# Performance work log

Measured on AMD Instinct MI355X. Metric: run time of the kernel, lower is better.

Reference implementation:

```python
import jax, jax.numpy as jnp
import numpy as np

B, S, H = 8, 1024, 1024
NH, HD = 16, 64
LN_EPS = 1e-12


def setup_inputs() -> dict:
    key = jax.random.key(0)
    ks = jax.random.split(key, 8)
    sd = 0.02
    return {
        "hidden_states": jax.random.normal(ks[0], (B, S, H), jnp.float32),
        "attention_mask": jnp.zeros((B, 1, 1, S), jnp.float32),
        "Wq": jax.random.normal(ks[1], (H, H), jnp.float32) * sd,
        "bq": jnp.zeros((H,), jnp.float32),
        "Wk": jax.random.normal(ks[2], (H, H), jnp.float32) * sd,
        "bk": jnp.zeros((H,), jnp.float32),
        "Wv": jax.random.normal(ks[3], (H, H), jnp.float32) * sd,
        "bv": jnp.zeros((H,), jnp.float32),
        "Wo": jax.random.normal(ks[4], (H, H), jnp.float32) * sd,
        "bo": jnp.zeros((H,), jnp.float32),
        "ln_gamma": jnp.ones((H,), jnp.float32),
        "ln_beta": jnp.zeros((H,), jnp.float32),
    }


def _heads(x):
    # [B,S,H] -> [B,NH,S,HD]
    return x.reshape(B, S, NH, HD).transpose(0, 2, 1, 3)


def reference(hidden_states, attention_mask, Wq, bq, Wk, bk, Wv, bv, Wo, bo, ln_gamma, ln_beta):
    # QKV projections (torch Linear: x @ W.T + b)
    q = _heads(hidden_states @ Wq.T + bq)
    k = _heads(hidden_states @ Wk.T + bk)
    v = _heads(hidden_states @ Wv.T + bv)
    # scaled dot-product attention with additive mask
    scores = jnp.einsum("bhqd,bhkd->bhqk", q, k) / np.sqrt(HD).astype(np.float32)
    scores = scores + attention_mask  # broadcast [B,1,1,S]
    probs = jax.nn.softmax(scores, axis=-1)
    ctx = jnp.einsum("bhqk,bhkd->bhqd", probs, v)
    ctx = ctx.transpose(0, 2, 1, 3).reshape(B, S, H)
    # output projection + residual + LayerNorm
    out = ctx @ Wo.T + bo
    x = out + hidden_states
    mu = jnp.mean(x, axis=-1, keepdims=True)
    var = jnp.var(x, axis=-1, keepdims=True)
    return (x - mu) * jax.lax.rsqrt(var + LN_EPS) * ln_gamma + ln_beta
```

## Files before the change

### kernel.cpp

```cpp
#include <hip/hip_runtime.h>
#include <stdint.h>

typedef __attribute__((ext_vector_type(8))) __bf16 bf16x8;
typedef __attribute__((ext_vector_type(8))) unsigned short ushortx8;
typedef __attribute__((ext_vector_type(4))) unsigned short ushortx4;
typedef __attribute__((ext_vector_type(4))) short short4v;
typedef __attribute__((ext_vector_type(4))) float floatx4;

#define LOG2E 1.4426950408889634f
#define QSCALE 0.18033688011112043f

#define ASYNC16(g, l) __builtin_amdgcn_global_load_lds( \
    (__attribute__((address_space(1))) void*)(g),       \
    (__attribute__((address_space(3))) void*)(l), 16, 0, 0)

__device__ __forceinline__ unsigned short f2bf(float f) {
    unsigned int u = __float_as_uint(f);
    u += 0x7fffu + ((u >> 16) & 1u);
    return (unsigned short)(u >> 16);
}
__device__ __forceinline__ float bf2f(unsigned short u) {
    return __uint_as_float((unsigned)u << 16);
}

__device__ __forceinline__ floatx4 mfma32(bf16x8 a, bf16x8 b, floatx4 c) {
    return __builtin_amdgcn_mfma_f32_16x16x32_bf16(a, b, c, 0, 0, 0);
}
__device__ __forceinline__ floatx4 mfma16(short4v a, short4v b, floatx4 c) {
    return __builtin_amdgcn_mfma_f32_16x16x16bf16_1k(a, b, c, 0, 0, 0);
}

__global__ __launch_bounds__(256) void cvt_all(
    const float* __restrict__ hidden,
    const float* __restrict__ Wq, const float* __restrict__ Wk,
    const float* __restrict__ Wv, const float* __restrict__ Wo,
    unsigned short* __restrict__ hid_bf,
    unsigned short* __restrict__ oqkv, unsigned short* __restrict__ oo)
{
    const float* src;
    unsigned short* dst;
    int i;
    if (blockIdx.x < 4096) {
        src = hidden; dst = hid_bf;
        i = blockIdx.x * 256 + threadIdx.x;
    } else {
        int blk = (blockIdx.x - 4096) >> 9;
        src = (blk == 0) ? Wq : (blk == 1) ? Wk : (blk == 2) ? Wv : Wo;
        dst = (blk == 3) ? oo : oqkv + (size_t)blk * 1048576;
        i = ((blockIdx.x - 4096) & 511) * 256 + threadIdx.x;
    }
    const float4* p = (const float4*)src + (size_t)i * 2;
    float4 a = p[0], b = p[1];
    ushortx8 o;
    o[0] = f2bf(a.x); o[1] = f2bf(a.y); o[2] = f2bf(a.z); o[3] = f2bf(a.w);
    o[4] = f2bf(b.x); o[5] = f2bf(b.y); o[6] = f2bf(b.z); o[7] = f2bf(b.w);
    *((ushortx8*)dst + i) = o;
}

template<bool SWAP>
__device__ __forceinline__ void kloop_dbuf(
    const unsigned short* __restrict__ Ag,
    const unsigned short* __restrict__ Wg,
    unsigned short As[2][8192], unsigned short Bs[2][8192],
    int wm, int wn, int l16, int quad, int t,
    floatx4 acc[4][4])
{
    const int t8 = t * 8;
#define SAx(bf_, i_, kt_) ASYNC16(Ag + (size_t)(i_) * 32 * 1024 + (kt_) * 64, &As[bf_][(i_) * 2048 + t8])
#define SBx(bf_, i_, kt_) ASYNC16(Wg + (size_t)(i_) * 32 * 1024 + (kt_) * 64, &Bs[bf_][(i_) * 2048 + t8])
#pragma unroll
    for (int i = 0; i < 4; i++) { SAx(0, i, 0); SBx(0, i, 0); }
    __syncthreads();

#pragma unroll 1
    for (int kt = 0; kt < 16; ++kt) {
        const int cur = kt & 1, nb = cur ^ 1;
        if (kt < 15) {
#pragma unroll
            for (int i = 0; i < 4; i++) { SAx(nb, i, kt + 1); SBx(nb, i, kt + 1); }
        }
#pragma unroll
        for (int s = 0; s < 2; s++) {
            int pb = ((s * 4 + quad) ^ (l16 & 7)) * 8;
            bf16x8 af[4], bfr[4];
#pragma unroll
            for (int mt = 0; mt < 4; mt++)
                af[mt] = *(const bf16x8*)(&As[cur][(wm + mt * 16 + l16) * 64 + pb]);
#pragma unroll
            for (int nt = 0; nt < 4; nt++)
                bfr[nt] = *(const bf16x8*)(&Bs[cur][(wn + nt * 16 + l16) * 64 + pb]);
            if (SWAP) {
#pragma unroll
                for (int ft = 0; ft < 4; ft++)
#pragma unroll
                    for (int st = 0; st < 4; st++)
                        acc[ft][st] = mfma32(bfr[ft], af[st], acc[ft][st]);
            } else {
#pragma unroll
                for (int mt = 0; mt < 4; mt++)
#pragma unroll
                    for (int nt = 0; nt < 4; nt++)
                        acc[mt][nt] = mfma32(af[mt], bfr[nt], acc[mt][nt]);
            }
        }
        __syncthreads();
    }
#undef SAx
#undef SBx
}

__global__ __launch_bounds__(256) void gemm_qkv(
    const unsigned short* __restrict__ A,
    const unsigned short* __restrict__ W,
    const float* __restrict__ bq, const float* __restrict__ bk, const float* __restrict__ bv,
    unsigned short* __restrict__ Qo, unsigned short* __restrict__ Ko,
    unsigned short* __restrict__ Vo)
{
    __shared__ unsigned short As[2][8192];
    __shared__ unsigned short Bs[2][12288];
    const int t = threadIdx.x;
    const int wave = t >> 6, lane = t & 63;
    const int quad = lane >> 4, l16 = lane & 15;
    const int wm = (wave >> 1) * 64;
    const int wn = (wave & 1) * 96;
    const int srow = t >> 3;
    const int scol = ((t & 7) ^ (srow & 7)) * 8;
    const int t8 = t * 8;

    const unsigned short* Ag = A + ((size_t)blockIdx.x * 128 + srow) * 1024 + scol;
    const unsigned short* Wg = W + ((size_t)blockIdx.y * 192 + srow) * 1024 + scol;

#define SA(bf_, i_, kt_) ASYNC16(Ag + (size_t)(i_) * 32 * 1024 + (kt_) * 64, &As[bf_][(i_) * 2048 + t8])
#define SB(bf_, i_, kt_) ASYNC16(Wg + (size_t)(i_) * 32 * 1024 + (kt_) * 64, &Bs[bf_][(i_) * 2048 + t8])

#pragma unroll
    for (int i = 0; i < 4; i++) SA(0, i, 0);
#pragma unroll
    for (int i = 0; i < 6; i++) SB(0, i, 0);
    __syncthreads();

    floatx4 acc[6][4] = {};

#pragma unroll 1
    for (int kt = 0; kt < 16; ++kt) {
        const int cur = kt & 1, nb = cur ^ 1;
        if (kt < 15) {
#pragma unroll
            for (int i = 0; i < 4; i++) SA(nb, i, kt + 1);
#pragma unroll
            for (int i = 0; i < 6; i++) SB(nb, i, kt + 1);
        }
#pragma unroll
        for (int s = 0; s < 2; s++) {
            int pb = ((s * 4 + quad) ^ (l16 & 7)) * 8;
            bf16x8 af[4], bfr[6];
#pragma unroll
            for (int mt = 0; mt < 4; mt++)
                af[mt] = *(const bf16x8*)(&As[cur][(wm + mt * 16 + l16) * 64 + pb]);
#pragma unroll
            for (int ft = 0; ft < 6; ft++)
                bfr[ft] = *(const bf16x8*)(&Bs[cur][(wn + ft * 16 + l16) * 64 + pb]);
#pragma unroll
            for (int ft = 0; ft < 6; ft++)
#pragma unroll
                for (int st = 0; st < 4; st++)
                    acc[ft][st] = mfma32(bfr[ft], af[st], acc[ft][st]);
        }
        __syncthreads();
    }
#undef SA
#undef SB

#pragma unroll
    for (int ft = 0; ft < 6; ++ft) {
        const int featg = blockIdx.y * 192 + wn + ft * 16 + quad * 4;
        const int mat = featg >> 10;
        const int fin = featg & 1023;
        if (mat < 2) {
            const float* bp = (mat == 0) ? bq : bk;
            unsigned short* op = (mat == 0) ? Qo : Ko;
            const float sc = (mat == 0) ? QSCALE : 1.0f;
            const float4 b4 = *(const float4*)(bp + fin);
            const int h = fin >> 6, d = fin & 63;
#pragma unroll
            for (int st = 0; st < 4; ++st) {
                const int sg = blockIdx.x * 128 + wm + st * 16 + l16;
                const int b = sg >> 10, s = sg & 1023;
                ushortx4 o4;
                o4[0] = f2bf((acc[ft][st][0] + b4.x) * sc);
                o4[1] = f2bf((acc[ft][st][1] + b4.y) * sc);
                o4[2] = f2bf((acc[ft][st][2] + b4.z) * sc);
                o4[3] = f2bf((acc[ft][st][3] + b4.w) * sc);
                *(ushortx4*)(op + (((size_t)(b * 16 + h) * 1024 + s) * 64 + d)) = o4;
            }
        } else {
            const float4 b4 = *(const float4*)(bv + fin);
#pragma unroll
            for (int r = 0; r < 4; ++r) {
                const int fr = fin + r;
                const int h = fr >> 6, d = fr & 63;
                const float bias = (r == 0) ? b4.x : (r == 1) ? b4.y : (r == 2) ? b4.z : b4.w;
#pragma unroll
                for (int st = 0; st < 4; ++st) {
                    const int sg = blockIdx.x * 128 + wm + st * 16 + l16;
                    const int b = sg >> 10, s = sg & 1023;
                    const int sp = (s & ~63) + (st >> 1) * 32 + (l16 >> 2) * 8 +
                                   (st & 1) * 4 + (l16 & 3);
                    Vo[((size_t)(b * 16 + h) * 64 + d) * 1024 + sp] = f2bf(acc[ft][st][r] + bias);
                }
            }
        }
    }
}

__global__ __launch_bounds__(256) void attn(
    const unsigned short* __restrict__ Q,
    const unsigned short* __restrict__ Kg,
    const unsigned short* __restrict__ Vt,
    const float* __restrict__ mask,
    unsigned short* __restrict__ ctx)
{
    __shared__ unsigned short Ks[64 * 64];
    __shared__ unsigned short Vs[64 * 64];
    __shared__ float Msall[1024];

    const int t = threadIdx.x;
    const int wave = t >> 6, lane = t & 63, quad = lane >> 4, l16 = lane & 15;
    const int s7 = l16 & 7;
    const int head = blockIdx.x;
    const int b = head >> 4, h = head & 15;
    const int q0 = blockIdx.y * 128;
    const unsigned short* Qh = Q + (size_t)head * 65536;
    const unsigned short* Kh = Kg + (size_t)head * 65536;
    const unsigned short* Vh = Vt + (size_t)head * 65536;

    const int srow = t >> 3;
    const int scol = ((t & 7) ^ (srow & 7)) * 8;

    {
        float4 m4 = *(const float4*)(mask + b * 1024 + t * 4);
        m4.x *= LOG2E; m4.y *= LOG2E; m4.z *= LOG2E; m4.w *= LOG2E;
        *(float4*)(Msall + t * 4) = m4;
    }

    bf16x8 qf[2][2];
#pragma unroll
    for (int qg = 0; qg < 2; qg++) {
        const unsigned short* qp = Qh + (size_t)(q0 + wave * 32 + qg * 16 + l16) * 64 + quad * 8;
        qf[qg][0] = *(const bf16x8*)(qp);
        qf[qg][1] = *(const bf16x8*)(qp + 32);
    }

    const short4v ones = {(short)0x3F80, (short)0x3F80, (short)0x3F80, (short)0x3F80};
    floatx4 sum_acc[2] = {};
    floatx4 o_acc[2][4] = {};

    for (int k0 = 0; k0 < 1024; k0 += 64) {
        __syncthreads();
#pragma unroll
        for (int i = 0; i < 2; i++) {
            ASYNC16(Kh + (size_t)(k0 + i * 32 + srow) * 64 + scol, Ks + i * 2048 + t * 8);
            ASYNC16(Vh + (size_t)(i * 32 + srow) * 1024 + k0 + scol, Vs + i * 2048 + t * 8);
        }
        __syncthreads();

        short4v pf0[4], pf1[4];
#pragma unroll
        for (int nt = 0; nt < 4; nt++) {
            int krow = nt * 16 + l16;
            bf16x8 kf0 = *(const bf16x8*)(Ks + krow * 64 + ((quad ^ s7) * 8));
            bf16x8 kf1 = *(const bf16x8*)(Ks + krow * 64 + (((4 + quad) ^ s7) * 8));
            floatx4 mk = *(const floatx4*)(Msall + k0 + nt * 16 + quad * 4);
            floatx4 z0 = mk;
            z0 = mfma32(kf0, qf[0][0], z0);
            z0 = mfma32(kf1, qf[0][1], z0);
            floatx4 z1 = mk;
            z1 = mfma32(kf0, qf[1][0], z1);
            z1 = mfma32(kf1, qf[1][1], z1);
#pragma unroll
            for (int r = 0; r < 4; r++) {
                pf0[nt][r] = (short)(__float_as_uint(exp2f(z0[r])) >> 16);
                pf1[nt][r] = (short)(__float_as_uint(exp2f(z1[r])) >> 16);
            }
            sum_acc[0] = mfma16(ones, pf0[nt], sum_acc[0]);
            sum_acc[1] = mfma16(ones, pf1[nt], sum_acc[1]);
        }

#pragma unroll
        for (int dt = 0; dt < 4; dt++) {
            int vrow = dt * 16 + l16;
            ushortx8 v01 = *(const ushortx8*)(Vs + vrow * 64 + ((quad ^ s7) * 8));
            ushortx8 v23 = *(const ushortx8*)(Vs + vrow * 64 + (((4 + quad) ^ s7) * 8));
            short4v vf0 = {(short)v01[0], (short)v01[1], (short)v01[2], (short)v01[3]};
            short4v vf1 = {(short)v01[4], (short)v01[5], (short)v01[6], (short)v01[7]};
            short4v vf2 = {(short)v23[0], (short)v23[1], (short)v23[2], (short)v23[3]};
            short4v vf3 = {(short)v23[4], (short)v23[5], (short)v23[6], (short)v23[7]};
            o_acc[0][dt] = mfma16(vf0, pf0[0], o_acc[0][dt]);
            o_acc[0][dt] = mfma16(vf1, pf0[1], o_acc[0][dt]);
            o_acc[0][dt] = mfma16(vf2, pf0[2], o_acc[0][dt]);
            o_acc[0][dt] = mfma16(vf3, pf0[3], o_acc[0][dt]);
            o_acc[1][dt] = mfma16(vf0, pf1[0], o_acc[1][dt]);
            o_acc[1][dt] = mfma16(vf1, pf1[1], o_acc[1][dt]);
            o_acc[1][dt] = mfma16(vf2, pf1[2], o_acc[1][dt]);
            o_acc[1][dt] = mfma16(vf3, pf1[3], o_acc[1][dt]);
        }
    }

#pragma unroll
    for (int qg = 0; qg < 2; qg++) {
        float inv_l = 1.0f / sum_acc[qg][0];
        int qrow = q0 + wave * 32 + qg * 16 + l16;
#pragma unroll
        for (int dt = 0; dt < 4; dt++) {
            ushortx4 o4;
#pragma unroll
            for (int r = 0; r < 4; r++) o4[r] = f2bf(o_acc[qg][dt][r] * inv_l);
            *(ushortx4*)(ctx + ((size_t)(b * 1024 + qrow)) * 1024 + h * 64 + dt * 16 + quad * 4) = o4;
        }
    }
}

__global__ __launch_bounds__(256) void gemm_proj(
    const unsigned short* __restrict__ A,
    const unsigned short* __restrict__ W,
    const float* __restrict__ bo,
    const unsigned short* __restrict__ resid,
    unsigned short* __restrict__ X)
{
    __shared__ unsigned short As[2][8192];
    __shared__ unsigned short Bs[2][8192];
    const int t = threadIdx.x;
    const int wave = t >> 6, lane = t & 63;
    const int quad = lane >> 4, l16 = lane & 15;
    const int wm = (wave >> 1) * 64, wn = (wave & 1) * 64;
    const int srow = t >> 3;
    const int scol = ((t & 7) ^ (srow & 7)) * 8;

    const unsigned short* Ag = A + ((size_t)blockIdx.x * 128 + srow) * 1024 + scol;
    const unsigned short* Wg = W + ((size_t)blockIdx.y * 128 + srow) * 1024 + scol;

    floatx4 acc[4][4] = {};
    kloop_dbuf<false>(Ag, Wg, As, Bs, wm, wn, l16, quad, t, acc);

#pragma unroll
    for (int nt = 0; nt < 4; nt++) {
        int gn = blockIdx.y * 128 + wn + nt * 16 + l16;
        float bias = bo[gn];
#pragma unroll
        for (int mt = 0; mt < 4; mt++) {
#pragma unroll
            for (int r = 0; r < 4; r++) {
                int gm = blockIdx.x * 128 + wm + mt * 16 + quad * 4 + r;
                size_t off = (size_t)gm * 1024 + gn;
                X[off] = f2bf(acc[mt][nt][r] + bias + bf2f(resid[off]));
            }
        }
    }
}

__global__ __launch_bounds__(256) void ln_k(const unsigned short* __restrict__ X,
                                            const float* __restrict__ g,
                                            const float* __restrict__ be,
                                            float* __restrict__ out)
{
    int row = blockIdx.x;
    int t = threadIdx.x;
    const unsigned short* xr = X + (size_t)row * 1024;
    ushortx4 xb = *(const ushortx4*)(xr + t * 4);
    float4 v;
    v.x = bf2f(xb[0]);
    v.y = bf2f(xb[1]);
    v.z = bf2f(xb[2]);
    v.w = bf2f(xb[3]);
    float s = v.x + v.y + v.z + v.w;
    float ss = v.x * v.x + v.y * v.y + v.z * v.z + v.w * v.w;
    for (int off = 1; off < 64; off <<= 1) {
        s += __shfl_xor(s, off);
        ss += __shfl_xor(ss, off);
    }
    __shared__ float red[8];
    int wave = t >> 6, lane = t & 63;
    if (lane == 0) { red[wave] = s; red[4 + wave] = ss; }
    __syncthreads();
    s = red[0] + red[1] + red[2] + red[3];
    ss = red[4] + red[5] + red[6] + red[7];
    float mu = s * (1.f / 1024.f);
    float var = ss * (1.f / 1024.f) - mu * mu;
    float inv = rsqrtf(var + 1e-12f);
    float4 gv = *(const float4*)(g + t * 4);
    float4 bv = *(const float4*)(be + t * 4);
    float4 o;
    o.x = (v.x - mu) * inv * gv.x + bv.x;
    o.y = (v.y - mu) * inv * gv.y + bv.y;
    o.z = (v.z - mu) * inv * gv.z + bv.z;
    o.w = (v.w - mu) * inv * gv.w + bv.w;
    *(float4*)(out + (size_t)row * 1024 + t * 4) = o;
}

extern "C" void kernel_launch(void* const* d_in, const int* in_sizes, int n_in,
                              void* d_out, int out_size, void* d_ws, size_t ws_size,
                              hipStream_t stream)
{
    const float* hidden = (const float*)d_in[0];
    const float* mask   = (const float*)d_in[1];
    const float* Wq = (const float*)d_in[2];
    const float* bq = (const float*)d_in[3];
    const float* Wk = (const float*)d_in[4];
    const float* bk = (const float*)d_in[5];
    const float* Wv = (const float*)d_in[6];
    const float* bv = (const float*)d_in[7];
    const float* Wo = (const float*)d_in[8];
    const float* bo = (const float*)d_in[9];
    const float* gamma = (const float*)d_in[10];
    const float* beta  = (const float*)d_in[11];
    float* out = (float*)d_out;

    char* ws = (char*)d_ws;
    unsigned short* hid_bf  = (unsigned short*)(ws + 0);
    unsigned short* wqkv_bf = (unsigned short*)(ws + 16777216);
    unsigned short* wo_bf   = (unsigned short*)(ws + 23068672);
    unsigned short* vt_bf   = (unsigned short*)(ws + 25165824);
    unsigned short* ctx_bf  = (unsigned short*)(ws + 41943040);
    unsigned short* q_bf    = (unsigned short*)(ws + 58720256);
    unsigned short* k_bf    = (unsigned short*)(ws + 75497472);
    unsigned short* x_bf    = (unsigned short*)(ws + 58720256);

    cvt_all<<<6144, 256, 0, stream>>>(hidden, Wq, Wk, Wv, Wo, hid_bf, wqkv_bf, wo_bf);

    gemm_qkv<<<dim3(64, 16), 256, 0, stream>>>(hid_bf, wqkv_bf, bq, bk, bv, q_bf, k_bf, vt_bf);
    attn<<<dim3(128, 8), 256, 0, stream>>>(q_bf, k_bf, vt_bf, mask, ctx_bf);
    gemm_proj<<<dim3(64, 8), 256, 0, stream>>>(ctx_bf, wo_bf, bo, hid_bf, x_bf);
    ln_k<<<8192, 256, 0, stream>>>(x_bf, gamma, beta, out);
}
```

Before: 296.4 us.

## Widen QKV GEMM tile to 128x256 with split B-buffer pipeline

The QKV projection kernel now computes a 128x256 output tile per block, processed as two 128-column halves. Each half has its own B shared buffer, and its load is interleaved with the MFMA work on the other half, while A stays double-buffered. The grid shrinks from 64x16 to 64x12 blocks, and launch bounds request two blocks per CU. The aim is more reuse of the A tile per global load with shared memory held to 64KB, at the cost of a larger accumulator array (32 floatx4 per thread) and register pressure that may limit occupancy.

Measured after the change: 269.8 us. -9.0%, faster.

```diff
diff --git a/kernel.cpp b/kernel.cpp
--- a/kernel.cpp
+++ b/kernel.cpp
@@ -109,7 +109,7 @@
 #undef SBx
 }
 
-__global__ __launch_bounds__(256) void gemm_qkv(
+__global__ __launch_bounds__(256, 2) void gemm_qkv(
     const unsigned short* __restrict__ A,
     const unsigned short* __restrict__ W,
     const float* __restrict__ bq, const float* __restrict__ bk, const float* __restrict__ bv,
@@ -117,54 +117,71 @@
     unsigned short* __restrict__ Vo)
 {
     __shared__ unsigned short As[2][8192];
-    __shared__ unsigned short Bs[2][12288];
+    __shared__ unsigned short Bs[2][8192];
     const int t = threadIdx.x;
     const int wave = t >> 6, lane = t & 63;
     const int quad = lane >> 4, l16 = lane & 15;
-    const int wm = (wave >> 1) * 64;
-    const int wn = (wave & 1) * 96;
+    const int wm = (wave >> 1) * 64, wn = (wave & 1) * 64;
     const int srow = t >> 3;
     const int scol = ((t & 7) ^ (srow & 7)) * 8;
     const int t8 = t * 8;
 
     const unsigned short* Ag = A + ((size_t)blockIdx.x * 128 + srow) * 1024 + scol;
-    const unsigned short* Wg = W + ((size_t)blockIdx.y * 192 + srow) * 1024 + scol;
-
-#define SA(bf_, i_, kt_) ASYNC16(Ag + (size_t)(i_) * 32 * 1024 + (kt_) * 64, &As[bf_][(i_) * 2048 + t8])
-#define SB(bf_, i_, kt_) ASYNC16(Wg + (size_t)(i_) * 32 * 1024 + (kt_) * 64, &Bs[bf_][(i_) * 2048 + t8])
-
-#pragma unroll
-    for (int i = 0; i < 4; i++) SA(0, i, 0);
-#pragma unroll
-    for (int i = 0; i < 6; i++) SB(0, i, 0);
+    const unsigned short* Wg = W + ((size_t)blockIdx.y * 256 + srow) * 1024 + scol;
+
+#define SA(bf_, i_, kt_) ASYNC16(Ag + (size_t)(i_) * 32768 + (kt_) * 64, &As[bf_][(i_) * 2048 + t8])
+#define SB(rb_, i_, rp_, kt_) ASYNC16(Wg + (size_t)(rp_) * 131072 + (size_t)(i_) * 32768 + (kt_) * 64, \
+                                      &Bs[rb_][(i_) * 2048 + t8])
+
+#pragma unroll
+    for (int i = 0; i < 4; i++) { SA(0, i, 0); SB(0, i, 0, 0); }
     __syncthreads();
 
-    floatx4 acc[6][4] = {};
+    floatx4 acc[2][4][4] = {};
 
 #pragma unroll 1
     for (int kt = 0; kt < 16; ++kt) {
         const int cur = kt & 1, nb = cur ^ 1;
-        if (kt < 15) {
-#pragma unroll
-            for (int i = 0; i < 4; i++) SA(nb, i, kt + 1);
-#pragma unroll
-            for (int i = 0; i < 6; i++) SB(nb, i, kt + 1);
-        }
+
+#pragma unroll
+        for (int i = 0; i < 4; i++) SB(1, i, 1, kt);
 #pragma unroll
         for (int s = 0; s < 2; s++) {
             int pb = ((s * 4 + quad) ^ (l16 & 7)) * 8;
-            bf16x8 af[4], bfr[6];
+            bf16x8 af[4], bfr[4];
 #pragma unroll
             for (int mt = 0; mt < 4; mt++)
                 af[mt] = *(const bf16x8*)(&As[cur][(wm + mt * 16 + l16) * 64 + pb]);
 #pragma unroll
-            for (int ft = 0; ft < 6; ft++)
-                bfr[ft] = *(const bf16x8*)(&Bs[cur][(wn + ft * 16 + l16) * 64 + pb]);
-#pragma unroll
-            for (int ft = 0; ft < 6; ft++)
+            for (int ft = 0; ft < 4; ft++)
+                bfr[ft] = *(const bf16x8*)(&Bs[0][(wn + ft * 16 + l16) * 64 + pb]);
+#pragma unroll
+            for (int ft = 0; ft < 4; ft++)
 #pragma unroll
                 for (int st = 0; st < 4; st++)
-                    acc[ft][st] = mfma32(bfr[ft], af[st], acc[ft][st]);
+                    acc[0][ft][st] = mfma32(bfr[ft], af[st], acc[0][ft][st]);
+        }
+        __syncthreads();
+
+        if (kt < 15) {
+#pragma unroll
+            for (int i = 0; i < 4; i++) { SB(0, i, 0, kt + 1); SA(nb, i, kt + 1); }
+        }
+#pragma unroll
+        for (int s = 0; s < 2; s++) {
+            int pb = ((s * 4 + quad) ^ (l16 & 7)) * 8;
+            bf16x8 af[4], bfr[4];
+#pragma unroll
+            for (int mt = 0; mt < 4; mt++)
+                af[mt] = *(const bf16x8*)(&As[cur][(wm + mt * 16 + l16) * 64 + pb]);
+#pragma unroll
+            for (int ft = 0; ft < 4; ft++)
+                bfr[ft] = *(const bf16x8*)(&Bs[1][(wn + ft * 16 + l16) * 64 + pb]);
+#pragma unroll
+            for (int ft = 0; ft < 4; ft++)
+#pragma unroll
+                for (int st = 0; st < 4; st++)
+                    acc[1][ft][st] = mfma32(bfr[ft], af[st], acc[1][ft][st]);
         }
         __syncthreads();
     }
@@ -172,8 +189,10 @@
 #undef SB
 
 #pragma unroll
-    for (int ft = 0; ft < 6; ++ft) {
-        const int featg = blockIdx.y * 192 + wn + ft * 16 + quad * 4;
+    for (int rp = 0; rp < 2; ++rp) {
+#pragma unroll
+    for (int ft = 0; ft < 4; ++ft) {
+        const int featg = blockIdx.y * 256 + rp * 128 + wn + ft * 16 + quad * 4;
         const int mat = featg >> 10;
         const int fin = featg & 1023;
         if (mat < 2) {
@@ -187,10 +206,10 @@
                 const int sg = blockIdx.x * 128 + wm + st * 16 + l16;
                 const int b = sg >> 10, s = sg & 1023;
                 ushortx4 o4;
-                o4[0] = f2bf((acc[ft][st][0] + b4.x) * sc);
-                o4[1] = f2bf((acc[ft][st][1] + b4.y) * sc);
-                o4[2] = f2bf((acc[ft][st][2] + b4.z) * sc);
-                o4[3] = f2bf((acc[ft][st][3] + b4.w) * sc);
+                o4[0] = f2bf((acc[rp][ft][st][0] + b4.x) * sc);
+                o4[1] = f2bf((acc[rp][ft][st][1] + b4.y) * sc);
+                o4[2] = f2bf((acc[rp][ft][st][2] + b4.z) * sc);
+                o4[3] = f2bf((acc[rp][ft][st][3] + b4.w) * sc);
                 *(ushortx4*)(op + (((size_t)(b * 16 + h) * 1024 + s) * 64 + d)) = o4;
             }
         } else {
@@ -206,10 +225,11 @@
                     const int b = sg >> 10, s = sg & 1023;
                     const int sp = (s & ~63) + (st >> 1) * 32 + (l16 >> 2) * 8 +
                                    (st & 1) * 4 + (l16 & 3);
-                    Vo[((size_t)(b * 16 + h) * 64 + d) * 1024 + sp] = f2bf(acc[ft][st][r] + bias);
+                    Vo[((size_t)(b * 16 + h) * 64 + d) * 1024 + sp] = f2bf(acc[rp][ft][st][r] + bias);
                 }
             }
         }
+    }
     }
 }
 
@@ -427,7 +447,7 @@
 
     cvt_all<<<6144, 256, 0, stream>>>(hidden, Wq, Wk, Wv, Wo, hid_bf, wqkv_bf, wo_bf);
 
-    gemm_qkv<<<dim3(64, 16), 256, 0, stream>>>(hid_bf, wqkv_bf, bq, bk, bv, q_bf, k_bf, vt_bf);
+    gemm_qkv<<<dim3(64, 12), 256, 0, stream>>>(hid_bf, wqkv_bf, bq, bk, bv, q_bf, k_bf, vt_bf);
     attn<<<dim3(128, 8), 256, 0, stream>>>(q_bf, k_bf, vt_bf, mask, ctx_bf);
     gemm_proj<<<dim3(64, 8), 256, 0, stream>>>(ctx_bf, wo_bf, bo, hid_bf, x_bf);
     ln_k<<<8192, 256, 0, stream>>>(x_bf, gamma, beta, out);
```
